# Kernel optimization log

Hardware: AMD Instinct MI355X
Metric: run time of the kernel (lower is better)

Reference implementation:

```python
import jax, jax.numpy as jnp
import numpy as np

EPS = 1e-8

def setup_inputs() -> dict:
    key = jax.random.key(0)
    ks = jax.random.split(key, 4)
    B, N, D = 16, 2048, 1024
    APP = 1024
    x = jax.random.normal(ks[0], (B, N, D), dtype=jnp.float32)
    mask = jax.random.uniform(ks[1], (N, B), dtype=jnp.float32)  # [N, B] per original
    Wp = jax.random.normal(ks[2], (1024, D), dtype=jnp.float32) * 0.02
    bp = jnp.zeros((1024,), dtype=jnp.float32)
    Wv = jax.random.normal(ks[3], (APP, D), dtype=jnp.float32) * 0.02
    bv = jnp.zeros((APP,), dtype=jnp.float32)
    return {"x": x, "mask": mask, "Wp": Wp, "bp": bp, "Wv": Wv, "bv": bv}

def reference(x, mask, Wp, bp, Wv, bv):
    # proj + ReLU: [B,N,1024]
    xp = jax.nn.relu(jnp.einsum('bnd,pd->bnp', x, Wp) + bp)
    # L2-normalize along feature dim (matches xp / (norm + eps))
    xp = xp / (jnp.linalg.norm(xp, axis=2, keepdims=True) + EPS)
    # mask: [N,B] -> [B,N] (transpose+reshape in original yields [B,1,N])
    m = mask.T  # [B, N]
    # att_i = sum_j m_j * <xp_i, xp_j> / sum_j m_j  == <xp_i, sum_j m_j xp_j> / sum_j m_j
    ws = jnp.einsum('bn,bnp->bp', m, xp)                # [B, 1024]
    att = jnp.einsum('bnp,bp->bn', xp, ws) / jnp.sum(m, axis=1, keepdims=True)  # [B, N]
    # value + ReLU: [B,N,APP]
    xv = jax.nn.relu(jnp.einsum('bnd,ad->bna', x, Wv) + bv)
    return att[:, :, None] * xv
```

## Files before the change

kernel.cpp:

```cpp
#include <hip/hip_runtime.h>

#define B_  16
#define N_  2048
#define D_  1024
#define P_  1024
#define M_  (B_*N_)

typedef __attribute__((ext_vector_type(8))) short bf16x8;
typedef __attribute__((ext_vector_type(4))) float f32x4;

__device__ __forceinline__ float bf2f(unsigned short u) {
    union { unsigned int i; float f; } v; v.i = ((unsigned int)u) << 16; return v.f;
}
__device__ __forceinline__ unsigned short f2bf(float f) {
    union { unsigned int i; float f; } v; v.f = f;
    unsigned int i = v.i;
    return (unsigned short)((i + 0x7FFFu + ((i >> 16) & 1u)) >> 16);
}

__device__ __forceinline__ void async_cp16(const void* g, void* s) {
    __builtin_amdgcn_global_load_lds((const __attribute__((address_space(1))) void*)g,
                                     (__attribute__((address_space(3))) void*)s,
                                     16, 0, 0);
}

__global__ void cvt_all_k(const float* __restrict__ x,  unsigned short* __restrict__ xb,
                          const float* __restrict__ Wp, unsigned short* __restrict__ Wpb,
                          const float* __restrict__ Wv, unsigned short* __restrict__ Wvb)
{
    const int stride = gridDim.x * 256 * 4;
    const int base = (blockIdx.x * 256 + threadIdx.x) * 4;
    for (int i = base; i < M_ * D_; i += stride) {
        float4 v = *(const float4*)(x + i);
        union { unsigned short u[4]; unsigned long long ll; } p;
        p.u[0]=f2bf(v.x); p.u[1]=f2bf(v.y); p.u[2]=f2bf(v.z); p.u[3]=f2bf(v.w);
        *(unsigned long long*)(xb + i) = p.ll;
    }
    for (int i = base; i < P_ * D_; i += stride) {
        float4 v = *(const float4*)(Wp + i);
        union { unsigned short u[4]; unsigned long long ll; } p;
        p.u[0]=f2bf(v.x); p.u[1]=f2bf(v.y); p.u[2]=f2bf(v.z); p.u[3]=f2bf(v.w);
        *(unsigned long long*)(Wpb + i) = p.ll;
    }
    for (int i = base; i < P_ * D_; i += stride) {
        float4 v = *(const float4*)(Wv + i);
        union { unsigned short u[4]; unsigned long long ll; } p;
        p.u[0]=f2bf(v.x); p.u[1]=f2bf(v.y); p.u[2]=f2bf(v.z); p.u[3]=f2bf(v.w);
        *(unsigned long long*)(Wvb + i) = p.ll;
    }
}

template<int MODE>
__global__ __launch_bounds__(256) void gemm_bf(const unsigned short* __restrict__ A,
                                               const unsigned short* __restrict__ W,
                                               const float* __restrict__ bias,
                                               const float* __restrict__ att,
                                               void* __restrict__ Cv)
{
    const int K = D_, BK = 64;
    __shared__ unsigned short As[128 * 64];
    __shared__ unsigned short Bs[128 * 64];

    const int id = blockIdx.x;
    const int bx = (id >> 3) & 7;
    const int by = ((id >> 6) << 3) | (id & 7);
    const int m0 = by * 128, p0 = bx * 128;

    const int wave = threadIdx.x >> 6, lane = threadIdx.x & 63;
    const int wr = wave >> 1, wc = wave & 1;

    const int srow = wave * 32 + (lane >> 3);
    const int scol = (((lane & 7) ^ (lane >> 3)) & 7) * 8;
    const unsigned short* ag = A + (size_t)(m0 + srow) * K + scol;
    const unsigned short* bg = W + (size_t)(p0 + srow) * K + scol;
    unsigned short* as = &As[srow * BK + (lane & 7) * 8];
    unsigned short* bs = &Bs[srow * BK + (lane & 7) * 8];

    f32x4 acc[4][4];
    #pragma unroll
    for (int i = 0; i < 4; i++)
        #pragma unroll
        for (int j = 0; j < 4; j++) acc[i][j] = (f32x4){0.f,0.f,0.f,0.f};

    const int lr = lane & 15, lq = lane >> 4;
    const unsigned short* ArR = &As[(wr * 64 + lr) * BK];
    const unsigned short* BrR = &Bs[(wc * 64 + lr) * BK];
    const int c0 = ((lq       ^ (lr & 7)) & 7) * 8;
    const int c1 = (((lq | 4) ^ (lr & 7)) & 7) * 8;

    for (int kb = 0; kb < K; kb += BK) {
        #pragma unroll
        for (int s = 0; s < 4; s++) {
            async_cp16(ag + (size_t)s * 8 * K + kb, as + s * 8 * BK);
            async_cp16(bg + (size_t)s * 8 * K + kb, bs + s * 8 * BK);
        }
        __syncthreads();
        bf16x8 af[2][4], bfr[2][4];
        #pragma unroll
        for (int i = 0; i < 4; i++) {
            af[0][i] = *(const bf16x8*)(ArR + i * 16 * BK + c0);
            af[1][i] = *(const bf16x8*)(ArR + i * 16 * BK + c1);
        }
        #pragma unroll
        for (int j = 0; j < 4; j++) {
            bfr[0][j] = *(const bf16x8*)(BrR + j * 16 * BK + c0);
            bfr[1][j] = *(const bf16x8*)(BrR + j * 16 * BK + c1);
        }
        #pragma unroll
        for (int h = 0; h < 2; h++)
            #pragma unroll
            for (int i = 0; i < 4; i++)
                #pragma unroll
                for (int j = 0; j < 4; j++)
                    acc[i][j] = __builtin_amdgcn_mfma_f32_16x16x32_bf16(af[h][i], bfr[h][j], acc[i][j], 0, 0, 0);
        __syncthreads();
    }

    const int crow0 = m0 + wr * 64 + lq * 4;
    const int ccol0 = p0 + wc * 64 + lr;
    #pragma unroll
    for (int i = 0; i < 4; i++) {
        float attv[4];
        if (MODE == 1) {
            #pragma unroll
            for (int v = 0; v < 4; v++) attv[v] = att[crow0 + i * 16 + v];
        }
        #pragma unroll
        for (int j = 0; j < 4; j++) {
            const int col = ccol0 + j * 16;
            const float bi = bias[col];
            #pragma unroll
            for (int v = 0; v < 4; v++) {
                const int row = crow0 + i * 16 + v;
                float val = fmaxf(acc[i][j][v] + bi, 0.0f);
                if (MODE == 0) ((unsigned short*)Cv)[(size_t)row * P_ + col] = f2bf(val);
                else           ((float*)Cv)[(size_t)row * P_ + col] = val * attv[v];
            }
        }
    }
}

template<int MODE>
__global__ __launch_bounds__(256) void gemm_f32(const float* __restrict__ A,
                                                const float* __restrict__ W,
                                                const float* __restrict__ bias,
                                                const float* __restrict__ att,
                                                void* __restrict__ Cv)
{
    const int K = D_, BK = 32;
    __shared__ float As[128 * 32];
    __shared__ float Bs[128 * 32];
    const int id = blockIdx.x;
    const int bx = (id >> 3) & 7;
    const int by = ((id >> 6) << 3) | (id & 7);
    const int m0 = by * 128, p0 = bx * 128;
    const int wave = threadIdx.x >> 6, lane = threadIdx.x & 63;
    const int wr = wave >> 1, wc = wave & 1;
    const int srow = wave * 32 + (lane >> 3);
    const int scol = (lane & 7) * 4;
    const float* ag = A + (size_t)(m0 + srow) * K + scol;
    const float* bg = W + (size_t)(p0 + srow) * K + scol;
    float* as = &As[srow * BK + scol];
    float* bs = &Bs[srow * BK + scol];
    f32x4 acc[4][4];
    #pragma unroll
    for (int i = 0; i < 4; i++)
        #pragma unroll
        for (int j = 0; j < 4; j++) acc[i][j] = (f32x4){0.f,0.f,0.f,0.f};
    const int lr = lane & 15, lq = lane >> 4;
    const float* Ar = &As[(wr * 64 + lr) * BK + lq * 8];
    const float* Br = &Bs[(wc * 64 + lr) * BK + lq * 8];
    for (int kb = 0; kb < K; kb += BK) {
        #pragma unroll
        for (int s = 0; s < 4; s++) {
            async_cp16(ag + (size_t)s * 8 * K + kb, as + s * 8 * BK);
            async_cp16(bg + (size_t)s * 8 * K + kb, bs + s * 8 * BK);
        }
        __syncthreads();
        bf16x8 af[4], bf[4];
        #pragma unroll
        for (int i = 0; i < 4; i++) {
            f32x4 a0 = *(const f32x4*)(Ar + i * 16 * BK);
            f32x4 a1 = *(const f32x4*)(Ar + i * 16 * BK + 4);
            #pragma unroll
            for (int e = 0; e < 4; e++) {
                union { float f; unsigned int u; } c;
                c.f = a0[e]; af[i][e]     = (short)(c.u >> 16);
                c.f = a1[e]; af[i][e + 4] = (short)(c.u >> 16);
            }
        }
        #pragma unroll
        for (int j = 0; j < 4; j++) {
            f32x4 b0 = *(const f32x4*)(Br + j * 16 * BK);
            f32x4 b1 = *(const f32x4*)(Br + j * 16 * BK + 4);
            #pragma unroll
            for (int e = 0; e < 4; e++) {
                union { float f; unsigned int u; } c;
                c.f = b0[e]; bf[j][e]     = (short)(c.u >> 16);
                c.f = b1[e]; bf[j][e + 4] = (short)(c.u >> 16);
            }
        }
        #pragma unroll
        for (int i = 0; i < 4; i++)
            #pragma unroll
            for (int j = 0; j < 4; j++)
                acc[i][j] = __builtin_amdgcn_mfma_f32_16x16x32_bf16(af[i], bf[j], acc[i][j], 0, 0, 0);
        __syncthreads();
    }
    const int crow0 = m0 + wr * 64 + lq * 4;
    const int ccol0 = p0 + wc * 64 + lr;
    #pragma unroll
    for (int i = 0; i < 4; i++) {
        float attv[4];
        if (MODE == 1) {
            #pragma unroll
            for (int v = 0; v < 4; v++) attv[v] = att[crow0 + i * 16 + v];
        }
        #pragma unroll
        for (int j = 0; j < 4; j++) {
            const int col = ccol0 + j * 16;
            const float bi = bias[col];
            #pragma unroll
            for (int v = 0; v < 4; v++) {
                const int row = crow0 + i * 16 + v;
                float val = fmaxf(acc[i][j][v] + bi, 0.0f);
                if (MODE == 0) ((unsigned short*)Cv)[(size_t)row * P_ + col] = f2bf(val);
                else           ((float*)Cv)[(size_t)row * P_ + col] = val * attv[v];
            }
        }
    }
}

__global__ __launch_bounds__(256) void fused_nc_k(const unsigned short* __restrict__ X1,
                                                  const float* __restrict__ mask,
                                                  float* __restrict__ inv,
                                                  float* __restrict__ wsv,
                                                  float* __restrict__ msum)
{
    __shared__ float accw[4][1024];
    __shared__ float mred[4];
    const int b = blockIdx.y, nc = blockIdx.x;
    const int wave = threadIdx.x >> 6, lane = threadIdx.x & 63;
    float acc[16];
    #pragma unroll
    for (int e = 0; e < 16; e++) acc[e] = 0.f;
    float msub = 0.f;
    const int rbase = b * N_ + nc * 64 + wave * 16;
    const int nbase = nc * 64 + wave * 16;
    for (int t = 0; t < 16; t++) {
        const int r = rbase + t;
        const unsigned short* row = X1 + (size_t)r * P_;
        bf16x8 u0 = *(const bf16x8*)(row + lane * 16);
        bf16x8 u1 = *(const bf16x8*)(row + lane * 16 + 8);
        float v[16], s = 0.f;
        #pragma unroll
        for (int e = 0; e < 8; e++) { v[e] = bf2f((unsigned short)u0[e]); s += v[e]*v[e]; }
        #pragma unroll
        for (int e = 0; e < 8; e++) { v[8+e] = bf2f((unsigned short)u1[e]); s += v[8+e]*v[8+e]; }
        #pragma unroll
        for (int off = 32; off > 0; off >>= 1) s += __shfl_down(s, off);
        s = __shfl(s, 0);
        const float iv = 1.f / (sqrtf(s) + 1e-8f);
        const float mk = mask[(nbase + t) * B_ + b];
        if (lane == 0) { inv[r] = iv; msub += mk; }
        const float w = mk * iv;
        #pragma unroll
        for (int e = 0; e < 16; e++) acc[e] += w * v[e];
    }
    #pragma unroll
    for (int e = 0; e < 16; e++) accw[wave][e * 64 + lane] = acc[e];
    if (lane == 0) mred[wave] = msub;
    __syncthreads();
    #pragma unroll
    for (int q = 0; q < 4; q++) {
        const int p = threadIdx.x * 4 + q;
        const int col = (p & 63) * 16 + (p >> 6);
        float ssum = accw[0][p] + accw[1][p] + accw[2][p] + accw[3][p];
        atomicAdd(&wsv[b * P_ + col], ssum);
    }
    if (threadIdx.x == 0) atomicAdd(&msum[b], mred[0] + mred[1] + mred[2] + mred[3]);
}

__global__ void att_k(const unsigned short* __restrict__ X1,
                      const float* __restrict__ wsvec,
                      const float* __restrict__ inv,
                      const float* __restrict__ msum,
                      float* __restrict__ att)
{
    const int r = blockIdx.x * 4 + (threadIdx.x >> 6);
    const int lane = threadIdx.x & 63;
    const int b = r >> 11;
    const unsigned short* row = X1 + (size_t)r * P_;
    const float* w = wsvec + b * P_;
    bf16x8 u0 = *(const bf16x8*)(row + lane * 8);
    bf16x8 u1 = *(const bf16x8*)(row + 512 + lane * 8);
    float s = 0.f;
    #pragma unroll
    for (int k = 0; k < 8; k++) s += bf2f((unsigned short)u0[k]) * w[lane * 8 + k];
    #pragma unroll
    for (int k = 0; k < 8; k++) s += bf2f((unsigned short)u1[k]) * w[512 + lane * 8 + k];
    #pragma unroll
    for (int off = 32; off > 0; off >>= 1) s += __shfl_down(s, off);
    if (lane == 0) att[r] = s * inv[r] / msum[b];
}

extern "C" void kernel_launch(void* const* d_in, const int* in_sizes, int n_in,
                              void* d_out, int out_size, void* d_ws, size_t ws_size,
                              hipStream_t stream)
{
    const float* x    = (const float*)d_in[0];
    const float* mask = (const float*)d_in[1];
    const float* Wp   = (const float*)d_in[2];
    const float* bp   = (const float*)d_in[3];
    const float* Wv   = (const float*)d_in[4];
    const float* bv   = (const float*)d_in[5];
    float* out = (float*)d_out;

    unsigned short* X1 = (unsigned short*)d_out;

    const size_t xb_bytes = (size_t)M_ * D_ * 2;
    const size_t wb_bytes = (size_t)P_ * D_ * 2;
    const size_t f_bytes  = 2 * (size_t)M_ * 4 + (size_t)B_ * P_ * 4 + 64;
    const bool big_ws = ws_size >= xb_bytes + 2 * wb_bytes + f_bytes;

    char* ws = (char*)d_ws;
    size_t off = 0;
    unsigned short *xb = nullptr, *Wpb = nullptr, *Wvb = nullptr;
    if (big_ws) {
        xb  = (unsigned short*)(ws + off); off += xb_bytes;
        Wpb = (unsigned short*)(ws + off); off += wb_bytes;
        Wvb = (unsigned short*)(ws + off); off += wb_bytes;
    }
    float* inv  = (float*)(ws + off); off += (size_t)M_ * 4;
    float* att  = (float*)(ws + off); off += (size_t)M_ * 4;
    float* wsv  = (float*)(ws + off); off += (size_t)B_ * P_ * 4;
    float* msum = (float*)(ws + off); off += 64;

    hipMemsetAsync(wsv, 0, (size_t)B_ * P_ * 4 + 64, stream);

    const int gblocks = (P_ / 128) * (M_ / 128);
    if (big_ws) {
        cvt_all_k<<<2048, 256, 0, stream>>>(x, xb, Wp, Wpb, Wv, Wvb);
        gemm_bf<0><<<gblocks, 256, 0, stream>>>(xb, Wpb, bp, nullptr, X1);
    } else {
        gemm_f32<0><<<gblocks, 256, 0, stream>>>(x, Wp, bp, nullptr, X1);
    }
    fused_nc_k<<<dim3(32, B_), 256, 0, stream>>>(X1, mask, inv, wsv, msum);
    att_k<<<M_ / 4, 256, 0, stream>>>(X1, wsv, inv, msum, att);
    if (big_ws) gemm_bf<1><<<gblocks, 256, 0, stream>>>(xb, Wvb, bv, att, out);
    else        gemm_f32<1><<<gblocks, 256, 0, stream>>>(x, Wv, bv, att, out);
}
```

Measured before the change: 419.2 us.

## Replace bf16 GEMM with 256x256-tile, 8-wave double-buffered pipelined kernel

```diff
diff --git a/kernel.cpp b/kernel.cpp
--- a/kernel.cpp
+++ b/kernel.cpp
@@ -51,90 +51,165 @@
 }
 
 template<int MODE>
-__global__ __launch_bounds__(256) void gemm_bf(const unsigned short* __restrict__ A,
-                                               const unsigned short* __restrict__ W,
-                                               const float* __restrict__ bias,
-                                               const float* __restrict__ att,
-                                               void* __restrict__ Cv)
-{
-    const int K = D_, BK = 64;
-    __shared__ unsigned short As[128 * 64];
-    __shared__ unsigned short Bs[128 * 64];
-
-    const int id = blockIdx.x;
-    const int bx = (id >> 3) & 7;
-    const int by = ((id >> 6) << 3) | (id & 7);
-    const int m0 = by * 128, p0 = bx * 128;
-
-    const int wave = threadIdx.x >> 6, lane = threadIdx.x & 63;
-    const int wr = wave >> 1, wc = wave & 1;
-
-    const int srow = wave * 32 + (lane >> 3);
-    const int scol = (((lane & 7) ^ (lane >> 3)) & 7) * 8;
-    const unsigned short* ag = A + (size_t)(m0 + srow) * K + scol;
-    const unsigned short* bg = W + (size_t)(p0 + srow) * K + scol;
-    unsigned short* as = &As[srow * BK + (lane & 7) * 8];
-    unsigned short* bs = &Bs[srow * BK + (lane & 7) * 8];
-
-    f32x4 acc[4][4];
-    #pragma unroll
-    for (int i = 0; i < 4; i++)
-        #pragma unroll
-        for (int j = 0; j < 4; j++) acc[i][j] = (f32x4){0.f,0.f,0.f,0.f};
-
-    const int lr = lane & 15, lq = lane >> 4;
-    const unsigned short* ArR = &As[(wr * 64 + lr) * BK];
-    const unsigned short* BrR = &Bs[(wc * 64 + lr) * BK];
+__global__ __launch_bounds__(512, 2) void gemm8p(const unsigned short* __restrict__ A,
+                                                 const unsigned short* __restrict__ W,
+                                                 const float* __restrict__ bias,
+                                                 const float* __restrict__ att,
+                                                 void* __restrict__ Cv)
+{
+    __shared__ unsigned short smem[65536];
+
+    const int id  = blockIdx.x;
+    const int xcd = id & 7, idx = id >> 3;
+    const int bx  = idx & 3;
+    const int by  = xcd * 16 + (idx >> 2);
+    const int m0  = by << 8, p0 = bx << 8;
+
+    const int t    = threadIdx.x;
+    const int lane = t & 63, wave = t >> 6;
+    const int wr   = wave >> 2, wc = wave & 3;
+    const int lr   = lane & 15, lq = lane >> 4;
+
+    const int aBase = (wr * 64 + lr) * 64;
+    const int bBase = (wc * 32 + lr) * 64;
     const int c0 = ((lq       ^ (lr & 7)) & 7) * 8;
     const int c1 = (((lq | 4) ^ (lr & 7)) & 7) * 8;
 
-    for (int kb = 0; kb < K; kb += BK) {
-        #pragma unroll
-        for (int s = 0; s < 4; s++) {
-            async_cp16(ag + (size_t)s * 8 * K + kb, as + s * 8 * BK);
-            async_cp16(bg + (size_t)s * 8 * K + kb, bs + s * 8 * BK);
-        }
-        __syncthreads();
-        bf16x8 af[2][4], bfr[2][4];
-        #pragma unroll
-        for (int i = 0; i < 4; i++) {
-            af[0][i] = *(const bf16x8*)(ArR + i * 16 * BK + c0);
-            af[1][i] = *(const bf16x8*)(ArR + i * 16 * BK + c1);
-        }
-        #pragma unroll
-        for (int j = 0; j < 4; j++) {
-            bfr[0][j] = *(const bf16x8*)(BrR + j * 16 * BK + c0);
-            bfr[1][j] = *(const bf16x8*)(BrR + j * 16 * BK + c1);
-        }
-        #pragma unroll
-        for (int h = 0; h < 2; h++)
-            #pragma unroll
-            for (int i = 0; i < 4; i++)
+    const int srowT = t >> 3;
+    const int slot8 = (t & 7) * 8;
+    const int lch8  = (((t & 7) ^ (srowT & 7)) & 7) * 8;
+    const unsigned short* Ag = A + ((size_t)m0 << 10) + lch8;
+    const unsigned short* Bg = W + ((size_t)p0 << 10) + lch8;
+
+    auto stageA = [&](int buf, int rb, int tt) {
+        const unsigned short* s = Ag + ((size_t)(rb + srowT) << 10) + (tt << 6);
+        async_cp16(s,                      smem + buf * 16384 + (rb + srowT) * 64 + slot8);
+        async_cp16(s + ((size_t)64 << 10), smem + buf * 16384 + (rb + 64 + srowT) * 64 + slot8);
+    };
+    auto stageB = [&](int buf, int rb, int tt) {
+        const unsigned short* s = Bg + ((size_t)(rb + srowT) << 10) + (tt << 6);
+        async_cp16(s,                      smem + 32768 + buf * 16384 + (rb + srowT) * 64 + slot8);
+        async_cp16(s + ((size_t)64 << 10), smem + 32768 + buf * 16384 + (rb + 64 + srowT) * 64 + slot8);
+    };
+
+    f32x4 acc[8][4];
+    #pragma unroll
+    for (int i = 0; i < 8; ++i)
+        #pragma unroll
+        for (int j = 0; j < 4; ++j) acc[i][j] = (f32x4){0.f, 0.f, 0.f, 0.f};
+
+    stageA(0, 0, 0); stageA(0, 128, 0); stageB(0, 0, 0); stageB(0, 128, 0);
+    stageA(1, 0, 1); stageA(1, 128, 1); stageB(1, 0, 1); stageB(1, 128, 1);
+    asm volatile("s_waitcnt vmcnt(8)" ::: "memory");
+    __builtin_amdgcn_sched_barrier(0);
+    __builtin_amdgcn_s_barrier();
+
+#define VMW4 do { asm volatile("s_waitcnt vmcnt(4)" ::: "memory"); \
+                  __builtin_amdgcn_sched_barrier(0); } while (0)
+#define NOVM ((void)0)
+#define PHASE(BUFC, MH, NH, STAGE_STMT, DO_VM) do {                                   \
+    bf16x8 afr[4][2], bfr[2][2];                                                      \
+    const unsigned short* Ab_ = smem + (BUFC) * 16384 + (MH) * 8192 + aBase;          \
+    const unsigned short* Bb_ = smem + 32768 + (BUFC) * 16384 + (NH) * 8192 + bBase;  \
+    _Pragma("unroll")                                                                 \
+    for (int i_ = 0; i_ < 4; ++i_) {                                                  \
+        afr[i_][0] = *(const bf16x8*)(Ab_ + i_ * 1024 + c0);                          \
+        afr[i_][1] = *(const bf16x8*)(Ab_ + i_ * 1024 + c1);                          \
+    }                                                                                 \
+    _Pragma("unroll")                                                                 \
+    for (int j_ = 0; j_ < 2; ++j_) {                                                  \
+        bfr[j_][0] = *(const bf16x8*)(Bb_ + j_ * 1024 + c0);                          \
+        bfr[j_][1] = *(const bf16x8*)(Bb_ + j_ * 1024 + c1);                          \
+    }                                                                                 \
+    STAGE_STMT;                                                                       \
+    __builtin_amdgcn_s_barrier();                                                     \
+    asm volatile("s_waitcnt lgkmcnt(0)" ::: "memory");                                \
+    __builtin_amdgcn_sched_barrier(0);                                                \
+    __builtin_amdgcn_s_setprio(1);                                                    \
+    _Pragma("unroll")                                                                 \
+    for (int h_ = 0; h_ < 2; ++h_)                                                    \
+        _Pragma("unroll")                                                             \
+        for (int i_ = 0; i_ < 4; ++i_)                                                \
+            _Pragma("unroll")                                                         \
+            for (int j_ = 0; j_ < 2; ++j_)                                            \
+                acc[(MH) * 4 + i_][(NH) * 2 + j_] =                                   \
+                    __builtin_amdgcn_mfma_f32_16x16x32_bf16(                          \
+                        afr[i_][h_], bfr[j_][h_],                                     \
+                        acc[(MH) * 4 + i_][(NH) * 2 + j_], 0, 0, 0);                  \
+    __builtin_amdgcn_s_setprio(0);                                                    \
+    DO_VM;                                                                            \
+    __builtin_amdgcn_s_barrier();                                                     \
+} while (0)
+
+    #pragma unroll 1
+    for (int it = 0; it < 8; ++it) {
+        const int t1 = 2 * it + 1;
+        const int t2 = (2 * it + 2) & 15;
+        const int t3 = (2 * it + 3) & 15;
+        PHASE(0, 0, 0, { if (it) stageA(1, 128, t1); }, NOVM);
+        PHASE(0, 1, 0, { if (it) stageB(1, 128, t1); }, NOVM);
+        PHASE(0, 0, 1, stageB(0, 0,   t2), NOVM);
+        PHASE(0, 1, 1, stageA(0, 0,   t2), VMW4);
+        PHASE(1, 0, 0, stageA(0, 128, t2), NOVM);
+        PHASE(1, 1, 0, stageB(0, 128, t2), NOVM);
+        PHASE(1, 0, 1, stageB(1, 0,   t3), NOVM);
+        PHASE(1, 1, 1, stageA(1, 0,   t3), VMW4);
+    }
+#undef PHASE
+#undef VMW4
+#undef NOVM
+
+    asm volatile("s_waitcnt vmcnt(0)" ::: "memory");
+    __syncthreads();
+
+    if (MODE == 0) {
+        float bi[4];
+        #pragma unroll
+        for (int nj = 0; nj < 4; ++nj)
+            bi[nj] = bias[p0 + ((nj >> 1) << 7) + wc * 32 + ((nj & 1) << 4) + lr];
+        unsigned short* Cp = (unsigned short*)Cv;
+        #pragma unroll
+        for (int mh = 0; mh < 2; ++mh) {
+            #pragma unroll
+            for (int i = 0; i < 4; ++i) {
+                const int rl = wr * 64 + i * 16 + lq * 4;
                 #pragma unroll
-                for (int j = 0; j < 4; j++)
-                    acc[i][j] = __builtin_amdgcn_mfma_f32_16x16x32_bf16(af[h][i], bfr[h][j], acc[i][j], 0, 0, 0);
-        __syncthreads();
-    }
-
-    const int crow0 = m0 + wr * 64 + lq * 4;
-    const int ccol0 = p0 + wc * 64 + lr;
-    #pragma unroll
-    for (int i = 0; i < 4; i++) {
-        float attv[4];
-        if (MODE == 1) {
-            #pragma unroll
-            for (int v = 0; v < 4; v++) attv[v] = att[crow0 + i * 16 + v];
-        }
-        #pragma unroll
-        for (int j = 0; j < 4; j++) {
-            const int col = ccol0 + j * 16;
-            const float bi = bias[col];
-            #pragma unroll
-            for (int v = 0; v < 4; v++) {
-                const int row = crow0 + i * 16 + v;
-                float val = fmaxf(acc[i][j][v] + bi, 0.0f);
-                if (MODE == 0) ((unsigned short*)Cv)[(size_t)row * P_ + col] = f2bf(val);
-                else           ((float*)Cv)[(size_t)row * P_ + col] = val * attv[v];
+                for (int nj = 0; nj < 4; ++nj) {
+                    const int colL = ((nj >> 1) << 7) + wc * 32 + ((nj & 1) << 4) + lr;
+                    #pragma unroll
+                    for (int v = 0; v < 4; ++v) {
+                        const float val = fmaxf(acc[mh * 4 + i][nj][v] + bi[nj], 0.f);
+                        smem[(rl + v) * 256 + colL] = f2bf(val);
+                    }
+                }
+            }
+            __syncthreads();
+            #pragma unroll
+            for (int pas = 0; pas < 8; ++pas) {
+                const int ix = pas * 512 + t;
+                const int row = ix >> 5, ch = ix & 31;
+                bf16x8 vv = *(const bf16x8*)(smem + row * 256 + ch * 8);
+                *(bf16x8*)(Cp + (size_t)(m0 + mh * 128 + row) * P_ + p0 + ch * 8) = vv;
+            }
+            __syncthreads();
+        }
+    } else {
+        float* Cp = (float*)Cv;
+        #pragma unroll
+        for (int mi = 0; mi < 8; ++mi) {
+            const int row = m0 + ((mi >> 2) << 7) + wr * 64 + ((mi & 3) << 4) + lq * 4;
+            float av[4];
+            #pragma unroll
+            for (int v = 0; v < 4; ++v) av[v] = att[row + v];
+            #pragma unroll
+            for (int nj = 0; nj < 4; ++nj) {
+                const int col = p0 + ((nj >> 1) << 7) + wc * 32 + ((nj & 1) << 4) + lr;
+                const float b0v = bias[col];
+                #pragma unroll
+                for (int v = 0; v < 4; ++v) {
+                    const float val = fmaxf(acc[mi][nj][v] + b0v, 0.f);
+                    Cp[(size_t)(row + v) * P_ + col] = val * av[v];
+                }
             }
         }
     }
@@ -338,15 +413,18 @@
 
     hipMemsetAsync(wsv, 0, (size_t)B_ * P_ * 4 + 64, stream);
 
-    const int gblocks = (P_ / 128) * (M_ / 128);
     if (big_ws) {
         cvt_all_k<<<2048, 256, 0, stream>>>(x, xb, Wp, Wpb, Wv, Wvb);
-        gemm_bf<0><<<gblocks, 256, 0, stream>>>(xb, Wpb, bp, nullptr, X1);
+        gemm8p<0><<<512, 512, 0, stream>>>(xb, Wpb, bp, nullptr, X1);
     } else {
+        const int gblocks = (P_ / 128) * (M_ / 128);
         gemm_f32<0><<<gblocks, 256, 0, stream>>>(x, Wp, bp, nullptr, X1);
     }
     fused_nc_k<<<dim3(32, B_), 256, 0, stream>>>(X1, mask, inv, wsv, msum);
     att_k<<<M_ / 4, 256, 0, stream>>>(X1, wsv, inv, msum, att);
-    if (big_ws) gemm_bf<1><<<gblocks, 256, 0, stream>>>(xb, Wvb, bv, att, out);
-    else        gemm_f32<1><<<gblocks, 256, 0, stream>>>(x, Wv, bv, att, out);
-}
+    if (big_ws) gemm8p<1><<<512, 512, 0, stream>>>(xb, Wvb, bv, att, out);
+    else {
+        const int gblocks = (P_ / 128) * (M_ / 128);
+        gemm_f32<1><<<gblocks, 256, 0, stream>>>(x, Wv, bv, att, out);
+    }
+}
```

Measured after the change: 415.3 us. No clear change (-0.9%).
